# Performance work log

Measured on AMD Instinct MI355X. Metric: run time of the kernel, lower is better.

Reference implementation:

```python
import jax, jax.numpy as jnp
import numpy as np

N_NODES = 50000
N_EDGES = 800000
IN_DIM = 128
NUM_HEADS = 8
OUT_DIM = 16  # per-head dim; NUM_HEADS*OUT_DIM == IN_DIM


def setup_inputs() -> dict:
    key = jax.random.key(0)
    ks = jax.random.split(key, 9)
    s = 1.0 / np.sqrt(IN_DIM)
    return {
        "h": jax.random.normal(ks[0], (N_NODES, IN_DIM), dtype=jnp.float32),
        "src": jax.random.randint(ks[1], (N_EDGES,), 0, N_NODES),
        "dst": jax.random.randint(ks[2], (N_EDGES,), 0, N_NODES),
        "WQ": jax.random.normal(ks[3], (IN_DIM, NUM_HEADS * OUT_DIM), dtype=jnp.float32) * s,
        "bQ": jnp.zeros((NUM_HEADS * OUT_DIM,), dtype=jnp.float32),
        "WK": jax.random.normal(ks[4], (IN_DIM, NUM_HEADS * OUT_DIM), dtype=jnp.float32) * s,
        "bK": jnp.zeros((NUM_HEADS * OUT_DIM,), dtype=jnp.float32),
        "WV": jax.random.normal(ks[5], (IN_DIM, NUM_HEADS * OUT_DIM), dtype=jnp.float32) * s,
        "bV": jnp.zeros((NUM_HEADS * OUT_DIM,), dtype=jnp.float32),
    }


def reference(h, src, dst, WQ, bQ, WK, bK, WV, bV):
    N = h.shape[0]
    # node projections -> [N, H, D]
    Q = (h @ WQ + bQ).reshape(N, NUM_HEADS, OUT_DIM)
    K = (h @ WK + bK).reshape(N, NUM_HEADS, OUT_DIM)
    V = (h @ WV + bV).reshape(N, NUM_HEADS, OUT_DIM)
    # edge-wise score: (K_src * Q_dst) summed over D, scaled by sqrt(D)
    inv_scale = 1.0 / np.sqrt(OUT_DIM)
    score = jnp.einsum("ehd,ehd->eh", K[src], Q[dst]) * inv_scale  # [E, H]
    score_soft = jnp.exp(jnp.clip(score, -5.0, 5.0))[..., None]    # [E, H, 1]
    # scatter-sum messages to destination nodes
    wV = jax.ops.segment_sum(V[src] * score_soft, dst, num_segments=N)  # [N, H, D]
    z = jax.ops.segment_sum(score_soft, dst, num_segments=N)            # [N, H, 1]
    return wV / (z + 1e-6)
```

## Files before the change

### kernel.cpp

```cpp
#include <hip/hip_runtime.h>
#include <hip/hip_bf16.h>

#define IN_DIM 128
#define NUM_HEADS 8
#define OUT_DIM 16

#define BKT_SHIFT 7
#define BKT_MASK 127
#define NB_MAX 512
#define SLAB_SHIFT 13

typedef unsigned int uint;
typedef unsigned short ushort;
using short8 = __attribute__((ext_vector_type(8))) short;
using f32x4  = __attribute__((ext_vector_type(4))) float;
using u32x2  = __attribute__((ext_vector_type(2))) uint;

__device__ inline uint bf16_rne(float x) {
    uint u = __float_as_uint(x);
    return (u + 0x7fffu + ((u >> 16) & 1u)) >> 16;
}

__global__ __launch_bounds__(256) void stage_wtrans(const int* __restrict__ src,
                                                    const int* __restrict__ dst,
                                                    int* __restrict__ bucketCursor,
                                                    uint* __restrict__ slab,
                                                    const float* __restrict__ WQ,
                                                    const float* __restrict__ WK,
                                                    const float* __restrict__ WV,
                                                    ushort* __restrict__ WT,
                                                    int nEdges, int nb, int sb) {
    const int t = threadIdx.x;

    if ((int)blockIdx.x >= sb) {
        int tid = (blockIdx.x - sb) * 256 + t;
        if (tid >= 384 * 16) return;
        int n = tid >> 4;
        int kg = tid & 15;
        const float* W = (n < 128) ? WQ : (n < 256) ? WK : WV;
        int c = n & 127;
        short8 o;
        #pragma unroll
        for (int j = 0; j < 8; ++j) {
            float v = W[(kg * 8 + j) * 128 + c];
            o[j] = (short)bf16_rne(v);
        }
        *(short8*)(WT + (size_t)n * 128 + kg * 8) = o;
        return;
    }

    __shared__ int cnt[4][NB_MAX];
    __shared__ int base[4][NB_MAX];
    const int wv = t >> 6;
    const int e0 = blockIdx.x * 2048;

    for (int i = t; i < 4 * NB_MAX; i += 256) ((int*)cnt)[i] = 0;
    __syncthreads();

    int myDst[8], mySrc[8];
    #pragma unroll
    for (int i = 0; i < 2; ++i) {
        int e = e0 + (i * 256 + t) * 4;
        if (e + 3 < nEdges) {
            int4 d4 = *(const int4*)(dst + e);
            int4 s4 = *(const int4*)(src + e);
            myDst[4*i+0] = d4.x; myDst[4*i+1] = d4.y; myDst[4*i+2] = d4.z; myDst[4*i+3] = d4.w;
            mySrc[4*i+0] = s4.x; mySrc[4*i+1] = s4.y; mySrc[4*i+2] = s4.z; mySrc[4*i+3] = s4.w;
        } else {
            #pragma unroll
            for (int k = 0; k < 4; ++k) {
                int ee = e + k;
                myDst[4*i+k] = (ee < nEdges) ? dst[ee] : -1;
                mySrc[4*i+k] = (ee < nEdges) ? src[ee] : 0;
            }
        }
    }
    #pragma unroll
    for (int i = 0; i < 8; ++i)
        if (myDst[i] >= 0) atomicAdd(&cnt[wv][myDst[i] >> BKT_SHIFT], 1);
    __syncthreads();

    for (int bb = t; bb < NB_MAX; bb += 256) {
        int c0 = cnt[0][bb], c1 = cnt[1][bb], c2 = cnt[2][bb], c3 = cnt[3][bb];
        int tot = c0 + c1 + c2 + c3;
        int gbase = (bb < nb && tot > 0) ? atomicAdd(&bucketCursor[bb], tot) : 0;
        base[0][bb] = gbase;
        base[1][bb] = gbase + c0;
        base[2][bb] = gbase + c0 + c1;
        base[3][bb] = gbase + c0 + c1 + c2;
    }
    __syncthreads();
    for (int i = t; i < 4 * NB_MAX; i += 256) ((int*)cnt)[i] = 0;
    __syncthreads();

    #pragma unroll
    for (int i = 0; i < 8; ++i) {
        int d = myDst[i];
        if (d >= 0) {
            int b = d >> BKT_SHIFT;
            int pos = base[wv][b] + atomicAdd(&cnt[wv][b], 1);
            if (pos < (1 << SLAB_SHIFT))
                slab[((size_t)b << SLAB_SHIFT) + pos] = (uint)mySrc[i] | ((uint)(d & BKT_MASK) << 17);
        }
    }
}

__global__ __launch_bounds__(256) void bucket_sort(const uint* __restrict__ slab,
                                                   const int* __restrict__ bucketCursor,
                                                   int* __restrict__ offsets,
                                                   int* __restrict__ srcSorted,
                                                   int nNodes, int nEdges, int nb) {
    __shared__ int cnt[128];
    __shared__ int sOutBase;
    const int b = blockIdx.x;
    const int t = threadIdx.x;
    const int count = bucketCursor[b];
    const uint* rec = slab + ((size_t)b << SLAB_SHIFT);

    if (t < 128) cnt[t] = 0;
    if (t >= 64 && t < 128) {
        int l = t - 64;
        int acc = 0;
        for (int i = l; i < b; i += 64) acc += bucketCursor[i];
        #pragma unroll
        for (int off = 32; off; off >>= 1) acc += __shfl_down(acc, off);
        if (l == 0) sOutBase = acc;
    }
    __syncthreads();

    for (int i = t; i < count; i += 256)
        atomicAdd(&cnt[rec[i] >> 17], 1);
    __syncthreads();

    const int outBase = sOutBase;
    if (t < 64) {
        int c0 = cnt[2 * t], c1 = cnt[2 * t + 1];
        int s = c0 + c1;
        int x = s;
        #pragma unroll
        for (int off = 1; off < 64; off <<= 1) { int y = __shfl_up(x, off); if (t >= off) x += y; }
        int prefix = x - s;
        int node0 = b << BKT_SHIFT;
        int g0 = node0 + 2 * t, g1 = node0 + 2 * t + 1;
        if (g0 < nNodes) offsets[g0] = outBase + prefix;
        if (g1 < nNodes) offsets[g1] = outBase + prefix + c0;
        cnt[2 * t] = prefix;
        cnt[2 * t + 1] = prefix + c0;
    }
    __syncthreads();

    for (int i = t; i < count; i += 256) {
        uint r = rec[i];
        int pos = atomicAdd(&cnt[r >> 17], 1);
        srcSorted[outBase + pos] = (int)(r & 0x1ffff);
    }
    if (b == 0 && t == 0) offsets[nNodes] = nEdges;
}

__global__ __launch_bounds__(64, 2) void proj_mfma(const float* __restrict__ h,
                                                   const short* __restrict__ WT,
                                                   const float* __restrict__ bQ,
                                                   const float* __restrict__ bK,
                                                   const float* __restrict__ bV,
                                                   uint* __restrict__ Qout,
                                                   uint* __restrict__ KVout,
                                                   int nNodes) {
    const int lane = threadIdx.x;
    const int lr = lane & 15;
    const int q = lane >> 4;
    const int node0 = (blockIdx.x >> 1) * 64;
    const int chalf = blockIdx.x & 1;

    short8 a[4][4];
    #pragma unroll
    for (int g = 0; g < 4; ++g) {
        const int row = node0 + g * 16 + lr;
        const bool ok = row < nNodes;
        #pragma unroll
        for (int ks = 0; ks < 4; ++ks) {
            short8 v = (short8)0;
            if (ok) {
                const float* p = h + (size_t)row * 128 + (ks * 4 + q) * 8;
                float4 f0 = *(const float4*)p;
                float4 f1 = *(const float4*)(p + 4);
                v[0] = (short)bf16_rne(f0.x); v[1] = (short)bf16_rne(f0.y);
                v[2] = (short)bf16_rne(f0.z); v[3] = (short)bf16_rne(f0.w);
                v[4] = (short)bf16_rne(f1.x); v[5] = (short)bf16_rne(f1.y);
                v[6] = (short)bf16_rne(f1.z); v[7] = (short)bf16_rne(f1.w);
            }
            a[g][ks] = v;
        }
    }

    const short8* WT8 = (const short8*)WT;

    #pragma unroll 1
    for (int cc = 0; cc < 4; ++cc) {
        const int c = chalf * 4 + cc;
        const int nq = c * 16 + lr;
        f32x4 aQ[4] = {{0,0,0,0},{0,0,0,0},{0,0,0,0},{0,0,0,0}};
        f32x4 aK[4] = {{0,0,0,0},{0,0,0,0},{0,0,0,0},{0,0,0,0}};
        f32x4 aV[4] = {{0,0,0,0},{0,0,0,0},{0,0,0,0},{0,0,0,0}};
        #pragma unroll
        for (int ks = 0; ks < 4; ++ks) {
            short8 bq = WT8[(size_t)nq * 16 + ks * 4 + q];
            short8 bk = WT8[(size_t)(nq + 128) * 16 + ks * 4 + q];
            short8 bv = WT8[(size_t)(nq + 256) * 16 + ks * 4 + q];
            #pragma unroll
            for (int g = 0; g < 4; ++g) {
                aQ[g] = __builtin_amdgcn_mfma_f32_16x16x32_bf16(a[g][ks], bq, aQ[g], 0, 0, 0);
                aK[g] = __builtin_amdgcn_mfma_f32_16x16x32_bf16(a[g][ks], bk, aK[g], 0, 0, 0);
                aV[g] = __builtin_amdgcn_mfma_f32_16x16x32_bf16(a[g][ks], bv, aV[g], 0, 0, 0);
            }
        }
        const float biasq = bQ[nq];
        const float biask = bK[nq];
        const float biasv = bV[nq];
        #pragma unroll
        for (int g = 0; g < 4; ++g) {
            #pragma unroll
            for (int r = 0; r < 4; ++r) {
                int node = node0 + g * 16 + q * 4 + r;
                float qval = aQ[g][r] + biasq;
                float qpart = __shfl_xor(qval, 1);
                if (node < nNodes) {
                    if ((lr & 1) == 0)
                        Qout[(size_t)node * 64 + (nq >> 1)] = bf16_rne(qval) | (bf16_rne(qpart) << 16);
                    KVout[(size_t)node * 128 + nq] =
                        bf16_rne(aK[g][r] + biask) | (bf16_rne(aV[g][r] + biasv) << 16);
                }
            }
        }
    }
}

__global__ __launch_bounds__(256) void agg_kernel(const int* __restrict__ offsets,
                                                  const int* __restrict__ srcSorted,
                                                  const uint* __restrict__ Q,
                                                  const uint4* __restrict__ KV,
                                                  float* __restrict__ out,
                                                  int nNodes) {
    int wid = (int)((blockIdx.x * (size_t)blockDim.x + threadIdx.x) >> 6);
    if (wid >= nNodes) return;
    const int lane = threadIdx.x & 63;
    const int li = lane & 31;
    const int hf = lane >> 5;
    const int beg = offsets[wid];
    const int end = offsets[wid + 1];

    u32x2 qp = __builtin_nontemporal_load((const u32x2*)(Q + (size_t)wid * 64) + li);
    f32x4 qv;
    qv.x = __uint_as_float(qp.x << 16);
    qv.y = __uint_as_float(qp.x & 0xffff0000u);
    qv.z = __uint_as_float(qp.y << 16);
    qv.w = __uint_as_float(qp.y & 0xffff0000u);

    f32x4 acc = {0.f, 0.f, 0.f, 0.f};
    float zacc = 0.f;

    auto compute = [&](uint4 u, float mask) {
        float k0 = __uint_as_float(u.x << 16), v0 = __uint_as_float(u.x & 0xffff0000u);
        float k1 = __uint_as_float(u.y << 16), v1 = __uint_as_float(u.y & 0xffff0000u);
        float k2 = __uint_as_float(u.z << 16), v2 = __uint_as_float(u.z & 0xffff0000u);
        float k3 = __uint_as_float(u.w << 16), v3 = __uint_as_float(u.w & 0xffff0000u);
        float p = k0 * qv.x + k1 * qv.y + k2 * qv.z + k3 * qv.w;
        p += __shfl_xor(p, 1);
        p += __shfl_xor(p, 2);
        float e = __expf(fminf(fmaxf(p * 0.25f, -5.0f), 5.0f)) * mask;
        acc.x += v0 * e; acc.y += v1 * e; acc.z += v2 * e; acc.w += v3 * e;
        zacc += e;
    };

    int j = beg;
    for (; j + 8 <= end; j += 8) {
        int sI[4];
        #pragma unroll
        for (int i = 0; i < 4; ++i) sI[i] = __builtin_nontemporal_load(srcSorted + j + 2 * i + hf);
        uint4 u[4];
        #pragma unroll
        for (int i = 0; i < 4; ++i) u[i] = KV[(size_t)sI[i] * 32 + li];
        #pragma unroll
        for (int i = 0; i < 4; ++i) compute(u[i], 1.f);
    }
    for (; j + 2 <= end; j += 2) {
        uint4 u = KV[(size_t)srcSorted[j + hf] * 32 + li];
        compute(u, 1.f);
    }
    if (j < end) {
        uint4 u = KV[(size_t)srcSorted[j] * 32 + li];
        compute(u, hf ? 0.f : 1.f);
    }

    acc.x += __shfl_xor(acc.x, 32);
    acc.y += __shfl_xor(acc.y, 32);
    acc.z += __shfl_xor(acc.z, 32);
    acc.w += __shfl_xor(acc.w, 32);
    zacc  += __shfl_xor(zacc, 32);

    if (hf == 0) {
        float inv = 1.0f / (zacc + 1e-6f);
        f32x4 o = {acc.x * inv, acc.y * inv, acc.z * inv, acc.w * inv};
        __builtin_nontemporal_store(o, (f32x4*)(out + (size_t)wid * 128) + li);
    }
}

extern "C" void kernel_launch(void* const* d_in, const int* in_sizes, int n_in,
                              void* d_out, int out_size, void* d_ws, size_t ws_size,
                              hipStream_t stream) {
    const float* h   = (const float*)d_in[0];
    const int*   src = (const int*)d_in[1];
    const int*   dst = (const int*)d_in[2];
    const float* WQ  = (const float*)d_in[3];
    const float* bQ  = (const float*)d_in[4];
    const float* WK  = (const float*)d_in[5];
    const float* bK  = (const float*)d_in[6];
    const float* WV  = (const float*)d_in[7];
    const float* bV  = (const float*)d_in[8];

    const int nNodes = in_sizes[0] / IN_DIM;
    const int nEdges = in_sizes[1];
    const int nb = (nNodes + (1 << BKT_SHIFT) - 1) >> BKT_SHIFT;

    float* out = (float*)d_out;
    const size_t nf = (size_t)nNodes * 128;

    uint*   Qw          = (uint*)d_ws;
    uint*   KVw         = Qw + (size_t)nNodes * 64;
    ushort* WTw         = (ushort*)(KVw + nf);
    int*    bucketCursor= (int*)(WTw + 384 * 128);
    int*    offsets     = bucketCursor + NB_MAX;
    int*    srcSorted   = offsets + (nNodes + 1);
    uint*   slab        = (uint*)(srcSorted + nEdges);

    (void)hipMemsetAsync(bucketCursor, 0, NB_MAX * sizeof(int), stream);

    int sb = (nEdges + 2047) / 2048;
    stage_wtrans<<<sb + 24, 256, 0, stream>>>(src, dst, bucketCursor, slab,
                                              WQ, WK, WV, WTw, nEdges, nb, sb);
    bucket_sort<<<nb, 256, 0, stream>>>(slab, bucketCursor, offsets, srcSorted, nNodes, nEdges, nb);

    int projBlocks = ((nNodes + 63) / 64) * 2;
    proj_mfma<<<projBlocks, 64, 0, stream>>>(h, (const short*)WTw, bQ, bK, bV, Qw, KVw, nNodes);

    int aggBlocks = (nNodes * 64 + 255) / 256;
    agg_kernel<<<aggBlocks, 256, 0, stream>>>(offsets, srcSorted, Qw, (const uint4*)KVw, out, nNodes);
}
```

Measured before the change: 122.1 us.

## Fuse bucket sort into projection kernel and use packed bf16 conversion

Merges the bucket_sort and proj_mfma kernels into one launch. The first nb blocks do the per-bucket counting sort and the rest do the MFMA projections, which saves a kernel launch and lets the two independent stages overlap. The sort part now runs with 64 threads per block instead of 256, so each bucket is processed with fewer threads. The manual round-to-nearest-even bf16 conversion is also replaced by the hardware v_cvt_pk_bf16_f32 instruction, which converts two floats per instruction.

```diff
diff --git a/kernel.cpp b/kernel.cpp
--- a/kernel.cpp
+++ b/kernel.cpp
@@ -16,9 +16,10 @@
 using f32x4  = __attribute__((ext_vector_type(4))) float;
 using u32x2  = __attribute__((ext_vector_type(2))) uint;
 
-__device__ inline uint bf16_rne(float x) {
-    uint u = __float_as_uint(x);
-    return (u + 0x7fffu + ((u >> 16) & 1u)) >> 16;
+__device__ inline uint cvt_pk_bf16(float a, float b) {
+    uint r;
+    asm("v_cvt_pk_bf16_f32 %0, %1, %2" : "=v"(r) : "v"(a), "v"(b));
+    return r;
 }
 
 __global__ __launch_bounds__(256) void stage_wtrans(const int* __restrict__ src,
@@ -39,13 +40,14 @@
         int kg = tid & 15;
         const float* W = (n < 128) ? WQ : (n < 256) ? WK : WV;
         int c = n & 127;
-        short8 o;
-        #pragma unroll
-        for (int j = 0; j < 8; ++j) {
-            float v = W[(kg * 8 + j) * 128 + c];
-            o[j] = (short)bf16_rne(v);
-        }
-        *(short8*)(WT + (size_t)n * 128 + kg * 8) = o;
+        union { short8 s; uint u[4]; } o;
+        #pragma unroll
+        for (int j = 0; j < 4; ++j) {
+            float v0 = W[(kg * 8 + 2 * j) * 128 + c];
+            float v1 = W[(kg * 8 + 2 * j + 1) * 128 + c];
+            o.u[j] = cvt_pk_bf16(v0, v1);
+        }
+        *(short8*)(WT + (size_t)n * 128 + kg * 8) = o.s;
         return;
     }
 
@@ -105,35 +107,40 @@
     }
 }
 
-__global__ __launch_bounds__(256) void bucket_sort(const uint* __restrict__ slab,
+__global__ __launch_bounds__(64, 2) void sort_proj(const uint* __restrict__ slab,
                                                    const int* __restrict__ bucketCursor,
                                                    int* __restrict__ offsets,
                                                    int* __restrict__ srcSorted,
+                                                   const float* __restrict__ h,
+                                                   const short* __restrict__ WT,
+                                                   const float* __restrict__ bQ,
+                                                   const float* __restrict__ bK,
+                                                   const float* __restrict__ bV,
+                                                   uint* __restrict__ Qout,
+                                                   uint* __restrict__ KVout,
                                                    int nNodes, int nEdges, int nb) {
-    __shared__ int cnt[128];
-    __shared__ int sOutBase;
-    const int b = blockIdx.x;
     const int t = threadIdx.x;
-    const int count = bucketCursor[b];
-    const uint* rec = slab + ((size_t)b << SLAB_SHIFT);
-
-    if (t < 128) cnt[t] = 0;
-    if (t >= 64 && t < 128) {
-        int l = t - 64;
+
+    if ((int)blockIdx.x < nb) {
+        __shared__ int cnt[128];
+        __shared__ int sOutBase;
+        const int b = blockIdx.x;
+        const int count = bucketCursor[b];
+        const uint* rec = slab + ((size_t)b << SLAB_SHIFT);
+
         int acc = 0;
-        for (int i = l; i < b; i += 64) acc += bucketCursor[i];
+        for (int i = t; i < b; i += 64) acc += bucketCursor[i];
         #pragma unroll
         for (int off = 32; off; off >>= 1) acc += __shfl_down(acc, off);
-        if (l == 0) sOutBase = acc;
-    }
-    __syncthreads();
-
-    for (int i = t; i < count; i += 256)
-        atomicAdd(&cnt[rec[i] >> 17], 1);
-    __syncthreads();
-
-    const int outBase = sOutBase;
-    if (t < 64) {
+        if (t == 0) sOutBase = acc;
+        cnt[t] = 0; cnt[t + 64] = 0;
+        __syncthreads();
+
+        for (int i = t; i < count; i += 64)
+            atomicAdd(&cnt[rec[i] >> 17], 1);
+        __syncthreads();
+
+        const int outBase = sOutBase;
         int c0 = cnt[2 * t], c1 = cnt[2 * t + 1];
         int s = c0 + c1;
         int x = s;
@@ -144,32 +151,26 @@
         int g0 = node0 + 2 * t, g1 = node0 + 2 * t + 1;
         if (g0 < nNodes) offsets[g0] = outBase + prefix;
         if (g1 < nNodes) offsets[g1] = outBase + prefix + c0;
+        __syncthreads();
         cnt[2 * t] = prefix;
         cnt[2 * t + 1] = prefix + c0;
-    }
-    __syncthreads();
-
-    for (int i = t; i < count; i += 256) {
-        uint r = rec[i];
-        int pos = atomicAdd(&cnt[r >> 17], 1);
-        srcSorted[outBase + pos] = (int)(r & 0x1ffff);
-    }
-    if (b == 0 && t == 0) offsets[nNodes] = nEdges;
-}
-
-__global__ __launch_bounds__(64, 2) void proj_mfma(const float* __restrict__ h,
-                                                   const short* __restrict__ WT,
-                                                   const float* __restrict__ bQ,
-                                                   const float* __restrict__ bK,
-                                                   const float* __restrict__ bV,
-                                                   uint* __restrict__ Qout,
-                                                   uint* __restrict__ KVout,
-                                                   int nNodes) {
-    const int lane = threadIdx.x;
+        __syncthreads();
+
+        for (int i = t; i < count; i += 64) {
+            uint r = rec[i];
+            int pos = atomicAdd(&cnt[r >> 17], 1);
+            srcSorted[outBase + pos] = (int)(r & 0x1ffff);
+        }
+        if (b == 0 && t == 0) offsets[nNodes] = nEdges;
+        return;
+    }
+
+    const int gw = blockIdx.x - nb;
+    const int lane = t;
     const int lr = lane & 15;
     const int q = lane >> 4;
-    const int node0 = (blockIdx.x >> 1) * 64;
-    const int chalf = blockIdx.x & 1;
+    const int node0 = (gw >> 1) * 64;
+    const int chalf = gw & 1;
 
     short8 a[4][4];
     #pragma unroll
@@ -178,17 +179,19 @@
         const bool ok = row < nNodes;
         #pragma unroll
         for (int ks = 0; ks < 4; ++ks) {
-            short8 v = (short8)0;
+            union { short8 s; uint u[4]; } v;
             if (ok) {
                 const float* p = h + (size_t)row * 128 + (ks * 4 + q) * 8;
                 float4 f0 = *(const float4*)p;
                 float4 f1 = *(const float4*)(p + 4);
-                v[0] = (short)bf16_rne(f0.x); v[1] = (short)bf16_rne(f0.y);
-                v[2] = (short)bf16_rne(f0.z); v[3] = (short)bf16_rne(f0.w);
-                v[4] = (short)bf16_rne(f1.x); v[5] = (short)bf16_rne(f1.y);
-                v[6] = (short)bf16_rne(f1.z); v[7] = (short)bf16_rne(f1.w);
+                v.u[0] = cvt_pk_bf16(f0.x, f0.y);
+                v.u[1] = cvt_pk_bf16(f0.z, f0.w);
+                v.u[2] = cvt_pk_bf16(f1.x, f1.y);
+                v.u[3] = cvt_pk_bf16(f1.z, f1.w);
+            } else {
+                v.s = (short8)0;
             }
-            a[g][ks] = v;
+            a[g][ks] = v.s;
         }
     }
 
@@ -225,9 +228,8 @@
                 float qpart = __shfl_xor(qval, 1);
                 if (node < nNodes) {
                     if ((lr & 1) == 0)
-                        Qout[(size_t)node * 64 + (nq >> 1)] = bf16_rne(qval) | (bf16_rne(qpart) << 16);
-                    KVout[(size_t)node * 128 + nq] =
-                        bf16_rne(aK[g][r] + biask) | (bf16_rne(aV[g][r] + biasv) << 16);
+                        Qout[(size_t)node * 64 + (nq >> 1)] = cvt_pk_bf16(qval, qpart);
+                    KVout[(size_t)node * 128 + nq] = cvt_pk_bf16(aK[g][r] + biask, aV[g][r] + biasv);
                 }
             }
         }
@@ -337,10 +339,11 @@
     int sb = (nEdges + 2047) / 2048;
     stage_wtrans<<<sb + 24, 256, 0, stream>>>(src, dst, bucketCursor, slab,
                                               WQ, WK, WV, WTw, nEdges, nb, sb);
-    bucket_sort<<<nb, 256, 0, stream>>>(slab, bucketCursor, offsets, srcSorted, nNodes, nEdges, nb);
-
-    int projBlocks = ((nNodes + 63) / 64) * 2;
-    proj_mfma<<<projBlocks, 64, 0, stream>>>(h, (const short*)WTw, bQ, bK, bV, Qw, KVw, nNodes);
+
+    int projWaves = ((nNodes + 63) / 64) * 2;
+    sort_proj<<<nb + projWaves, 64, 0, stream>>>(slab, bucketCursor, offsets, srcSorted,
+                                                 h, (const short*)WTw, bQ, bK, bV,
+                                                 Qw, KVw, nNodes, nEdges, nb);
 
     int aggBlocks = (nNodes * 64 + 255) / 256;
     agg_kernel<<<aggBlocks, 256, 0, stream>>>(offsets, srcSorted, Qw, (const uint4*)KVw, out, nNodes);
```

Measured after the change: 118.3 us. 3.1% less time.
